# Performance work log

Measured on AMD Instinct MI355X. Metric: run time of the kernel, lower is better.

Reference implementation:

```python
import jax, jax.numpy as jnp
import numpy as np

BN_EPS = 1e-5


def setup_inputs() -> dict:
    key = jax.random.key(0)
    ks = jax.random.split(key, 12)
    B, C, N = 8, 256, 2048
    s = 1.0 / np.sqrt(C)
    x = jax.random.normal(ks[0], (B, C, N), dtype=jnp.float32)
    gamma = jnp.ones((C,), jnp.float32)
    beta = jnp.zeros((C,), jnp.float32)
    Wq = jax.random.normal(ks[1], (C, C), jnp.float32) * s
    bq = jnp.zeros((C,), jnp.float32)
    Wk = jax.random.normal(ks[2], (C, C), jnp.float32) * s
    bk = jnp.zeros((C,), jnp.float32)
    Wv = jax.random.normal(ks[3], (C, C), jnp.float32) * s
    bv = jnp.zeros((C,), jnp.float32)
    Wp = jax.random.normal(ks[4], (C, C), jnp.float32) * s
    bp = jnp.zeros((C,), jnp.float32)
    return {"x": x, "gamma": gamma, "beta": beta, "Wq": Wq, "bq": bq,
            "Wk": Wk, "bk": bk, "Wv": Wv, "bv": bv, "Wp": Wp, "bp": bp}


def reference(x, gamma, beta, Wq, bq, Wk, bk, Wv, bv, Wp, bp):
    B, C, N = x.shape
    # BatchNorm1d (training-mode batch stats): normalize per channel over (B, N)
    mean = jnp.mean(x, axis=(0, 2), keepdims=True)            # [1,C,1]
    var = jnp.mean(jnp.square(x - mean), axis=(0, 2), keepdims=True)
    h = (x - mean) * jax.lax.rsqrt(var + BN_EPS)
    h = h * gamma[None, :, None] + beta[None, :, None]
    # 1x1 Conv1d projections == per-position channel GEMMs
    q = jnp.einsum('oc,bcn->bno', Wq, h) + bq[None, None, :]  # [B,N,C]
    k = jnp.einsum('oc,bcn->bon', Wk, h) + bk[None, :, None]  # [B,C,N]
    v = jnp.einsum('oc,bcn->bno', Wv, h) + bv[None, None, :]  # [B,N,C]
    scale = jnp.asarray(C, x.dtype) ** -0.5
    w = jnp.einsum('bnc,bcm->bnm', q, k) * scale              # [B,N,N]
    w = jax.nn.softmax(w, axis=-1)
    h = jnp.einsum('bnm,bmc->bnc', w, v)                      # [B,N,C]
    out = jnp.einsum('oc,bnc->bon', Wp, h) + bp[None, :, None]  # [B,C,N]
    return x + out
```

## Files before the change

### kernel.cpp

```cpp
#include <hip/hip_runtime.h>
#include <hip/hip_fp16.h>

typedef _Float16 f16x8 __attribute__((ext_vector_type(8)));
typedef _Float16 f16x4 __attribute__((ext_vector_type(4)));
typedef float f32x4 __attribute__((ext_vector_type(4)));
typedef float f32x16 __attribute__((ext_vector_type(16)));

#define MFMA16(a, b, c) __builtin_amdgcn_mfma_f32_16x16x32_f16(a, b, c, 0, 0, 0)
#define MFMA32(a, b, c) __builtin_amdgcn_mfma_f32_32x32x16_f16(a, b, c, 0, 0, 0)

__device__ __forceinline__ void gload_lds16(const _Float16* g, void* l) {
    __builtin_amdgcn_global_load_lds(
        (const __attribute__((address_space(1))) void*)g,
        (__attribute__((address_space(3))) void*)l, 16, 0, 0);
}

__device__ __forceinline__ unsigned pkh(float a, float b) {
    typedef __fp16 fp16v2 __attribute__((ext_vector_type(2)));
    fp16v2 h = __builtin_amdgcn_cvt_pkrtz(a, b);
    return __builtin_bit_cast(unsigned, h);
}

__device__ __forceinline__ float fexp2(float x) {
#if __has_builtin(__builtin_amdgcn_exp2f)
    return __builtin_amdgcn_exp2f(x);
#else
    return exp2f(x);
#endif
}

__global__ __launch_bounds__(256) void prep_w_kernel(
    const float* __restrict__ Wq, const float* __restrict__ Wk,
    const float* __restrict__ Wv, const float* __restrict__ Wp,
    const float* __restrict__ bq, const float* __restrict__ bk,
    _Float16* __restrict__ out, float* __restrict__ bqk)
{
    int bid = blockIdx.x;
    int t = threadIdx.x;
    if (bid == 1024) {
        bqk[t]       = bq[t];
        bqk[256 + t] = bk[t];
        return;
    }
    int i = bid * 256 + t;
    int w = i >> 16, j = i & 65535;
    const float* src = (w == 0) ? Wq : (w == 1) ? Wk : (w == 2) ? Wv : Wp;
    out[i] = (_Float16)src[j];
}

__global__ __launch_bounds__(256) void bn_stats_kernel(
    const float* __restrict__ x, const float* __restrict__ gamma,
    const float* __restrict__ beta, float* __restrict__ scale,
    float* __restrict__ shift)
{
    int c = blockIdx.x, t = threadIdx.x;
    float s = 0.f, ss = 0.f;
    for (int b = 0; b < 8; ++b) {
        const float* p = x + ((size_t)b * 256 + c) * 2048;
        for (int n = t * 4; n < 2048; n += 1024) {
            float4 v = *(const float4*)(p + n);
            s  += v.x + v.y + v.z + v.w;
            ss += v.x*v.x + v.y*v.y + v.z*v.z + v.w*v.w;
        }
    }
    for (int off = 32; off > 0; off >>= 1) {
        s  += __shfl_down(s,  off, 64);
        ss += __shfl_down(ss, off, 64);
    }
    __shared__ float rs[4], rss[4];
    int w = t >> 6;
    if ((t & 63) == 0) { rs[w] = s; rss[w] = ss; }
    __syncthreads();
    if (t == 0) {
        float S  = rs[0] + rs[1] + rs[2] + rs[3];
        float SS = rss[0] + rss[1] + rss[2] + rss[3];
        float mean = S * (1.f / 16384.f);
        float var  = SS * (1.f / 16384.f) - mean * mean;
        float rstd = rsqrtf(var + 1e-5f);
        float sc = rstd * gamma[c];
        scale[c] = sc;
        shift[c] = beta[c] - mean * sc;
    }
}

__global__ __launch_bounds__(256) void norm_t_kernel(
    const float* __restrict__ x, const float* __restrict__ scale,
    const float* __restrict__ shift, _Float16* __restrict__ ht)
{
    __shared__ float tile[64][65];
    int t = threadIdx.x;
    int b = blockIdx.z, c0 = blockIdx.y * 64, n0 = blockIdx.x * 64;
    int nl = t & 63, cq = t >> 6;
#pragma unroll
    for (int r = 0; r < 16; ++r) {
        int cl = cq * 16 + r;
        float v = x[((size_t)b * 256 + c0 + cl) * 2048 + n0 + nl];
        tile[cl][nl] = v * scale[c0 + cl] + shift[c0 + cl];
    }
    __syncthreads();
    int cl2 = t & 63, nq = t >> 6;
#pragma unroll
    for (int r = 0; r < 16; ++r) {
        int nl2 = nq * 16 + r;
        ht[((size_t)b * 2048 + n0 + nl2) * 256 + c0 + cl2] = (_Float16)tile[cl2][nl2];
    }
}

template<int BN, int WGM, int WGN, typename OT, bool BIAS_I, bool RES>
__global__ __launch_bounds__(256, 3) void gemm_nt(
    const _Float16* __restrict__ Aall, long strideA,
    const _Float16* __restrict__ Ball, long strideB,
    const float* __restrict__ bias,
    const float* __restrict__ resid, long strideR,
    OT* __restrict__ Call, long strideC, int Nn)
{
    constexpr int BM = 128;
    constexpr int WR = BM / WGM;
    constexpr int WC = BN / WGN;
    constexpr int FM = WR / 16, FN = WC / 16;
    constexpr int BUFSZ = 8192 + BN * 64;
    constexpr int NI = 8 + BN / 16;
    constexpr int PW = NI / 4;

    int b = blockIdx.z;
    const _Float16* A  = Aall + (size_t)b * strideA;
    const _Float16* Bm = Ball + (size_t)b * strideB;
    OT* C = Call + (size_t)b * strideC;
    int i0 = blockIdx.y * BM, j0 = blockIdx.x * BN;

    __shared__ __align__(16) char lds[2 * BUFSZ];

    int t = threadIdx.x, lane = t & 63, w = t >> 6;
    int lr = lane & 15, lg = lane >> 4;
    int wm = w % WGM, wn = w / WGM;

    int soff = (lane >> 2) * 256 + (((lane & 3) ^ ((lane >> 3) & 3))) * 8;
    int lgx16 = ((lg ^ ((lr >> 1) & 3))) * 16;

    f32x4 acc[FM][FN] = {};

    auto stage = [&](int kk, int buf) {
#pragma unroll
        for (int i = 0; i < PW; ++i) {
            int u = w * PW + i;
            if (u < 8)
                gload_lds16(A + (size_t)(i0 + u * 16) * 256 + kk * 32 + soff,
                            lds + buf * BUFSZ + u * 1024);
            else
                gload_lds16(Bm + (size_t)(j0 + (u - 8) * 16) * 256 + kk * 32 + soff,
                            lds + buf * BUFSZ + 8192 + (u - 8) * 1024);
        }
    };

    stage(0, 0);
    __syncthreads();
    int buf = 0;
#pragma unroll
    for (int kk = 0; kk < 8; ++kk) {
        if (kk + 1 < 8) stage(kk + 1, buf ^ 1);
        const char* ab = lds + buf * BUFSZ;
        const char* bb = ab + 8192;
        f16x8 af[FM], bf[FN];
#pragma unroll
        for (int f = 0; f < FM; ++f)
            af[f] = *(const f16x8*)(ab + (wm * WR + f * 16 + lr) * 64 + lgx16);
#pragma unroll
        for (int f = 0; f < FN; ++f)
            bf[f] = *(const f16x8*)(bb + (wn * WC + f * 16 + lr) * 64 + lgx16);
        __builtin_amdgcn_s_setprio(1);
#pragma unroll
        for (int fm = 0; fm < FM; ++fm)
#pragma unroll
            for (int fn = 0; fn < FN; ++fn)
                acc[fm][fn] = MFMA16(af[fm], bf[fn], acc[fm][fn]);
        __builtin_amdgcn_s_setprio(0);
        __syncthreads();
        buf ^= 1;
    }
#pragma unroll
    for (int fm = 0; fm < FM; ++fm)
#pragma unroll
        for (int fn = 0; fn < FN; ++fn)
#pragma unroll
            for (int rr = 0; rr < 4; ++rr) {
                int row = i0 + wm * WR + fm * 16 + lg * 4 + rr;
                int col = j0 + wn * WC + fn * 16 + lr;
                float vv = acc[fm][fn][rr] + (BIAS_I ? bias[row] : bias[col]);
                if (RES) vv += resid[(size_t)b * strideR + (size_t)row * Nn + col];
                C[(size_t)row * Nn + col] = (OT)vv;
            }
}

__global__ __launch_bounds__(256, 2) void attn2_kernel(
    const _Float16* __restrict__ qk, const _Float16* __restrict__ vb,
    _Float16* __restrict__ Opart, float* __restrict__ mpart,
    float* __restrict__ lpart, int nsp, int mspan)
{
    int id = blockIdx.x;
    int b = id & 7;
    int rest = id >> 3;
    int qblk = rest & 15, sp = rest >> 4;
    int m_base = sp * mspan;
    int T = mspan >> 5;

    __shared__ __align__(16) char lds[66560];

    int t = threadIdx.x, ln = t & 63, w = t >> 6;
    int col = ln & 31, hi = ln >> 5;

    const _Float16* kg = qk + (size_t)b * 1048576 + 256;
    const _Float16* vg = vb + (size_t)b * 524288;

    int hsw = ((ln & 1) ^ ((ln >> 3) & 1));
    int koffs[4], voffs[4];
#pragma unroll
    for (int i = 0; i < 4; ++i) {
        int n = w * 4 + i;
        koffs[i] = (ln >> 1) * 512 + hsw * 8 + n * 16;
        voffs[i] = (((n & 7) * 32 + (ln >> 1)) * 2048) + ((n >> 3) * 16) + hsw * 8;
    }
    int frd = col * 32 + ((hi ^ ((col >> 2) & 1))) * 16;

    f16x8 qf[16];
    {
        const _Float16* qp = qk + ((size_t)b * 2048 + qblk * 128 + w * 32 + col) * 512 + hi * 8;
#pragma unroll
        for (int ks = 0; ks < 16; ++ks) {
            f16x8 v = *(const f16x8*)(qp + ks * 16);
#pragma unroll
            for (int e = 0; e < 8; ++e) v[e] = v[e] * (_Float16)0.09016844f;
            qf[ks] = v;
        }
    }

    f32x16 oacc[8] = {};
    float m_run = -1e30f, l_run = 0.f;

#pragma unroll
    for (int i = 0; i < 4; ++i) {
        int n = w * 4 + i;
        gload_lds16(kg + (size_t)m_base * 512 + koffs[i], lds + n * 1024);
        gload_lds16(vg + m_base + voffs[i], lds + 16384 + n * 1024);
    }
    __syncthreads();

    int buf = 0;
    for (int tt = 0; tt < T; ++tt) {
        if (tt + 1 < T) {
            int m0 = m_base + (tt + 1) * 32;
            char* kb = lds + (buf ^ 1) * 32768;
#pragma unroll
            for (int i = 0; i < 4; ++i) {
                int n = w * 4 + i;
                gload_lds16(kg + (size_t)m0 * 512 + koffs[i], kb + n * 1024);
                gload_lds16(vg + m0 + voffs[i], kb + 16384 + n * 1024);
            }
        }
        const char* kbase = lds + buf * 32768;
        const char* vbase = kbase + 16384;

        f32x16 s0 = {}, s1 = {};
        __builtin_amdgcn_s_setprio(1);
#pragma unroll
        for (int ks = 0; ks < 16; ks += 2) {
            f16x8 kf0 = *(const f16x8*)(kbase + ks * 1024 + frd);
            f16x8 kf1 = *(const f16x8*)(kbase + (ks + 1) * 1024 + frd);
            s0 = MFMA32(kf0, qf[ks], s0);
            s1 = MFMA32(kf1, qf[ks + 1], s1);
        }
        __builtin_amdgcn_s_setprio(0);
        f32x16 sacc = s0 + s1;

        float a0 = fmaxf(sacc[0], sacc[8]),  a1 = fmaxf(sacc[1], sacc[9]);
        float a2 = fmaxf(sacc[2], sacc[10]), a3 = fmaxf(sacc[3], sacc[11]);
        float a4 = fmaxf(sacc[4], sacc[12]), a5 = fmaxf(sacc[5], sacc[13]);
        float a6 = fmaxf(sacc[6], sacc[14]), a7 = fmaxf(sacc[7], sacc[15]);
        a0 = fmaxf(a0, a4); a1 = fmaxf(a1, a5); a2 = fmaxf(a2, a6); a3 = fmaxf(a3, a7);
        a0 = fmaxf(a0, a2); a1 = fmaxf(a1, a3);
        float rm = fmaxf(a0, a1);
        rm = fmaxf(rm, __shfl_xor(rm, 32, 64));

        if (__any(rm > m_run + 8.0f)) {
            float mnew = fmaxf(m_run, rm);
            float alpha = fexp2(m_run - mnew);
            l_run *= alpha;
#pragma unroll
            for (int dt = 0; dt < 8; ++dt) oacc[dt] *= alpha;
            m_run = mnew;
        }

        float pv_[16];
#pragma unroll
        for (int i = 0; i < 16; ++i) pv_[i] = fexp2(sacc[i] - m_run);
        float q0s = (pv_[0] + pv_[8])  + (pv_[1] + pv_[9]);
        float q1s = (pv_[2] + pv_[10]) + (pv_[3] + pv_[11]);
        float q2s = (pv_[4] + pv_[12]) + (pv_[5] + pv_[13]);
        float q3s = (pv_[6] + pv_[14]) + (pv_[7] + pv_[15]);
        float psum = (q0s + q1s) + (q2s + q3s);
        psum += __shfl_xor(psum, 32, 64);
        l_run += psum;

        unsigned W0[2], W1[2], W2[2], W3[2];
        W0[0] = pkh(pv_[0],  pv_[1]);  W0[1] = pkh(pv_[2],  pv_[3]);
        W1[0] = pkh(pv_[4],  pv_[5]);  W1[1] = pkh(pv_[6],  pv_[7]);
        W2[0] = pkh(pv_[8],  pv_[9]);  W2[1] = pkh(pv_[10], pv_[11]);
        W3[0] = pkh(pv_[12], pv_[13]); W3[1] = pkh(pv_[14], pv_[15]);

        __builtin_amdgcn_s_setprio(1);
#pragma unroll
        for (int j = 0; j < 2; ++j) {
            unsigned A0 = j ? W2[0] : W0[0], A1 = j ? W2[1] : W0[1];
            unsigned B0 = j ? W3[0] : W1[0], B1 = j ? W3[1] : W1[1];
            unsigned sx0 = hi ? A0 : B0, sx1 = hi ? A1 : B1;
            unsigned r0 = __shfl_xor(sx0, 32, 64), r1 = __shfl_xor(sx1, 32, 64);
            union { unsigned u[4]; f16x8 v; } pf;
            pf.u[0] = hi ? r0 : A0; pf.u[1] = hi ? r1 : A1;
            pf.u[2] = hi ? B0 : r0; pf.u[3] = hi ? B1 : r1;
#pragma unroll
            for (int dt = 0; dt < 8; ++dt) {
                f16x8 vf = *(const f16x8*)(vbase + j * 8192 + dt * 1024 + frd);
                oacc[dt] = MFMA32(vf, pf.v, oacc[dt]);
            }
        }
        __builtin_amdgcn_s_setprio(0);

        __syncthreads();
        buf ^= 1;
    }

    __syncthreads();
    _Float16* tr = (_Float16*)(lds + w * 16640);
    float invl = 1.0f / l_run;
#pragma unroll
    for (int dt = 0; dt < 8; ++dt)
#pragma unroll
        for (int g = 0; g < 4; ++g) {
            f16x4 q4;
#pragma unroll
            for (int e = 0; e < 4; ++e) q4[e] = (_Float16)(oacc[dt][g * 4 + e] * invl);
            int d0 = dt * 32 + g * 8 + 4 * hi;
            *(f16x4*)(tr + col * 260 + d0) = q4;
        }
    size_t region = ((size_t)((sp * 8 + b) * 16 + qblk)) * 32768;
    int rrow = ln >> 1, h = ln & 1;
    const _Float16* srcr = tr + rrow * 260 + h * 128;
    _Float16* dstr = Opart + region + (size_t)(w * 32 + rrow) * 256 + h * 128;
#pragma unroll
    for (int i = 0; i < 16; ++i)
        *(f16x8*)(dstr + i * 8) = *(const f16x8*)(srcr + i * 8);

    if (hi == 0) {
        int qi = w * 32 + col;
        int base = ((sp * 8 + b) * 16 + qblk) * 128 + qi;
        mpart[base] = m_run;
        lpart[base] = l_run;
    }
}

__global__ __launch_bounds__(256) void combine2_kernel(
    const _Float16* __restrict__ Opart, const float* __restrict__ mpart,
    const float* __restrict__ lpart, _Float16* __restrict__ abuf, int nsp)
{
    int id = blockIdx.x;
    int b = id & 7, qb = (id >> 3) & 15, dh = id >> 7;
    int t = threadIdx.x;
    __shared__ float cf[4][128];
    if (t < 128) {
        float m[4], l[4], mx = -1e30f;
        for (int sp = 0; sp < nsp; ++sp) {
            int base = ((sp * 8 + b) * 16 + qb) * 128 + t;
            m[sp] = mpart[base]; l[sp] = lpart[base];
            mx = fmaxf(mx, m[sp]);
        }
        float Wt = 0.f;
        for (int sp = 0; sp < nsp; ++sp) {
            float wv = l[sp] * fexp2(m[sp] - mx);
            cf[sp][t] = wv; Wt += wv;
        }
        float inv = 1.0f / Wt;
        for (int sp = 0; sp < nsp; ++sp) cf[sp][t] *= inv;
    }
    __syncthreads();
    size_t rb = ((size_t)(b * 16 + qb)) * 32768;
#pragma unroll
    for (int i = 0; i < 8; ++i) {
        int flat = i * 2048 + t * 8;
        int qi = flat >> 7, dl = flat & 127;
        float acc[8] = {};
        for (int sp = 0; sp < nsp; ++sp) {
            f16x8 v = *(const f16x8*)(Opart + (size_t)sp * 4194304 + rb +
                                      (size_t)qi * 256 + dh * 128 + dl);
            float c = cf[sp][qi];
#pragma unroll
            for (int e = 0; e < 8; ++e) acc[e] += c * (float)v[e];
        }
        f16x8 r;
#pragma unroll
        for (int e = 0; e < 8; ++e) r[e] = (_Float16)acc[e];
        *(f16x8*)(abuf + ((size_t)b * 2048 + qb * 128 + qi) * 256 + dh * 128 + dl) = r;
    }
}

extern "C" void kernel_launch(void* const* d_in, const int* in_sizes, int n_in,
                              void* d_out, int out_size, void* d_ws, size_t ws_size,
                              hipStream_t stream) {
    const float* x     = (const float*)d_in[0];
    const float* gamma = (const float*)d_in[1];
    const float* beta  = (const float*)d_in[2];
    const float* Wq    = (const float*)d_in[3];
    const float* bq    = (const float*)d_in[4];
    const float* Wk    = (const float*)d_in[5];
    const float* bk    = (const float*)d_in[6];
    const float* Wv    = (const float*)d_in[7];
    const float* bv    = (const float*)d_in[8];
    const float* Wp    = (const float*)d_in[9];
    const float* bp    = (const float*)d_in[10];
    float* out = (float*)d_out;

    char* ws = (char*)d_ws;
    float* scale = (float*)ws;
    float* shift = (float*)(ws + 1024);
    float* bqk   = (float*)(ws + 2048);
    float* mpart = (float*)(ws + 4096);
    float* lpart = (float*)(ws + 1052672);
    _Float16* wbf   = (_Float16*)(ws + 2101248);
    _Float16* Wvh   = wbf + 131072;
    _Float16* Wph   = wbf + 196608;
    _Float16* ht    = (_Float16*)(ws + 2625536);
    _Float16* qkbuf = (_Float16*)(ws + 11014144);
    _Float16* vbuf  = (_Float16*)(ws + 27791360);
    _Float16* Opart = (_Float16*)(ws + 36179968);
    _Float16* abuf  = ht;

    int nsp = (ws_size >= (size_t)36179968 + 4u * 8388608u) ? 4 : 2;
    int mspan = 2048 / nsp;

    const long SB = 524288;

    prep_w_kernel<<<1025, 256, 0, stream>>>(Wq, Wk, Wv, Wp, bq, bk, wbf, bqk);
    bn_stats_kernel<<<256, 256, 0, stream>>>(x, gamma, beta, scale, shift);
    norm_t_kernel<<<dim3(32, 4, 8), 256, 0, stream>>>(x, scale, shift, ht);
    gemm_nt<128, 2, 2, _Float16, false, false><<<dim3(4, 16, 8), 256, 0, stream>>>(
        ht, SB, wbf, 0, bqk, nullptr, 0, qkbuf, 1048576, 512);
    gemm_nt<64, 4, 1, _Float16, true, false><<<dim3(32, 2, 8), 256, 0, stream>>>(
        Wvh, 0, ht, SB, bv, nullptr, 0, vbuf, SB, 2048);
    attn2_kernel<<<128 * nsp, 256, 0, stream>>>(qkbuf, vbuf, Opart, mpart, lpart,
                                                nsp, mspan);
    combine2_kernel<<<256, 256, 0, stream>>>(Opart, mpart, lpart, abuf, nsp);
    gemm_nt<64, 4, 1, float, true, true><<<dim3(32, 2, 8), 256, 0, stream>>>(
        Wph, 0, abuf, SB, bp, x, SB, out, SB, 2048);
}
```

Before: 112.1 us.

## Rework attention pipeline: register-staged V, smaller LDS, 3 blocks/CU, up to 6 KV splits

The attention kernel now double-buffers only K in LDS through async global-to-LDS loads. V is prefetched into registers and written to a single LDS buffer after a barrier. This cuts LDS from 66.5KB to 48KB so launch bounds can target 3 blocks per CU, and the KV range can be split 6 ways when workspace allows. The PV MFMAs are interleaved with the exp computation for each half, the LDS swizzle is dropped, and the epilogue is done in two halves to fit the smaller LDS. Risks include bank conflicts from removing the swizzle, register pressure under the 3-block bound, and extra combine work with more splits.

```diff
diff --git a/kernel.cpp b/kernel.cpp
--- a/kernel.cpp
+++ b/kernel.cpp
@@ -191,19 +191,20 @@
             }
 }
 
-__global__ __launch_bounds__(256, 2) void attn2_kernel(
+__global__ __launch_bounds__(256, 3) void attn3_kernel(
     const _Float16* __restrict__ qk, const _Float16* __restrict__ vb,
     _Float16* __restrict__ Opart, float* __restrict__ mpart,
-    float* __restrict__ lpart, int nsp, int mspan)
+    float* __restrict__ lpart, int nsp)
 {
     int id = blockIdx.x;
     int b = id & 7;
     int rest = id >> 3;
     int qblk = rest & 15, sp = rest >> 4;
-    int m_base = sp * mspan;
-    int T = mspan >> 5;
-
-    __shared__ __align__(16) char lds[66560];
+    int t0 = (64 * sp) / nsp;
+    int t1 = (64 * (sp + 1)) / nsp;
+    int Tn = t1 - t0;
+
+    __shared__ __align__(16) char lds[49152];
 
     int t = threadIdx.x, ln = t & 63, w = t >> 6;
     int col = ln & 31, hi = ln >> 5;
@@ -211,15 +212,14 @@
     const _Float16* kg = qk + (size_t)b * 1048576 + 256;
     const _Float16* vg = vb + (size_t)b * 524288;
 
-    int hsw = ((ln & 1) ^ ((ln >> 3) & 1));
     int koffs[4], voffs[4];
 #pragma unroll
     for (int i = 0; i < 4; ++i) {
         int n = w * 4 + i;
-        koffs[i] = (ln >> 1) * 512 + hsw * 8 + n * 16;
-        voffs[i] = (((n & 7) * 32 + (ln >> 1)) * 2048) + ((n >> 3) * 16) + hsw * 8;
-    }
-    int frd = col * 32 + ((hi ^ ((col >> 2) & 1))) * 16;
+        koffs[i] = (ln >> 1) * 512 + (ln & 1) * 8 + n * 16;
+        voffs[i] = (((n & 7) * 32 + (ln >> 1)) * 2048) + ((n >> 3) * 16) + (ln & 1) * 8;
+    }
+    int frd = col * 32 + hi * 16;
 
     f16x8 qf[16];
     {
@@ -236,28 +236,41 @@
     f32x16 oacc[8] = {};
     float m_run = -1e30f, l_run = 0.f;
 
-#pragma unroll
-    for (int i = 0; i < 4; ++i) {
-        int n = w * 4 + i;
-        gload_lds16(kg + (size_t)m_base * 512 + koffs[i], lds + n * 1024);
-        gload_lds16(vg + m_base + voffs[i], lds + 16384 + n * 1024);
-    }
-    __syncthreads();
+    char* K0 = lds;
+    char* V  = lds + 32768;
+
+    {
+#pragma unroll
+        for (int i = 0; i < 4; ++i)
+            gload_lds16(kg + (size_t)(t0 * 32) * 512 + koffs[i], K0 + (w * 4 + i) * 1024);
+        int4 vr[4];
+#pragma unroll
+        for (int i = 0; i < 4; ++i)
+            vr[i] = *(const int4*)(vg + t0 * 32 + voffs[i]);
+#pragma unroll
+        for (int i = 0; i < 4; ++i)
+            *(int4*)(V + (w * 4 + i) * 1024 + ln * 16) = vr[i];
+        asm volatile("s_waitcnt vmcnt(0) lgkmcnt(0)" ::: "memory");
+        __builtin_amdgcn_sched_barrier(0);
+        if (Tn > 1) {
+#pragma unroll
+            for (int i = 0; i < 4; ++i)
+                gload_lds16(kg + (size_t)((t0 + 1) * 32) * 512 + koffs[i],
+                            K0 + 16384 + (w * 4 + i) * 1024);
+        }
+        __builtin_amdgcn_s_barrier();
+    }
 
     int buf = 0;
-    for (int tt = 0; tt < T; ++tt) {
-        if (tt + 1 < T) {
-            int m0 = m_base + (tt + 1) * 32;
-            char* kb = lds + (buf ^ 1) * 32768;
-#pragma unroll
-            for (int i = 0; i < 4; ++i) {
-                int n = w * 4 + i;
-                gload_lds16(kg + (size_t)m0 * 512 + koffs[i], kb + n * 1024);
-                gload_lds16(vg + m0 + voffs[i], kb + 16384 + n * 1024);
-            }
-        }
-        const char* kbase = lds + buf * 32768;
-        const char* vbase = kbase + 16384;
+    for (int tt = 0; tt < Tn; ++tt) {
+        int4 vr[4];
+        if (tt + 1 < Tn) {
+            int m0 = (t0 + tt + 1) * 32;
+#pragma unroll
+            for (int i = 0; i < 4; ++i)
+                vr[i] = *(const int4*)(vg + m0 + voffs[i]);
+        }
+        const char* kbase = lds + buf * 16384;
 
         f32x16 s0 = {}, s1 = {};
         __builtin_amdgcn_s_setprio(1);
@@ -289,65 +302,92 @@
             m_run = mnew;
         }
 
-        float pv_[16];
-#pragma unroll
-        for (int i = 0; i < 16; ++i) pv_[i] = fexp2(sacc[i] - m_run);
-        float q0s = (pv_[0] + pv_[8])  + (pv_[1] + pv_[9]);
-        float q1s = (pv_[2] + pv_[10]) + (pv_[3] + pv_[11]);
-        float q2s = (pv_[4] + pv_[12]) + (pv_[5] + pv_[13]);
-        float q3s = (pv_[6] + pv_[14]) + (pv_[7] + pv_[15]);
-        float psum = (q0s + q1s) + (q2s + q3s);
+        float pv0[8];
+#pragma unroll
+        for (int i = 0; i < 8; ++i) pv0[i] = fexp2(sacc[i] - m_run);
+        unsigned W0[2], W1[2];
+        W0[0] = pkh(pv0[0], pv0[1]); W0[1] = pkh(pv0[2], pv0[3]);
+        W1[0] = pkh(pv0[4], pv0[5]); W1[1] = pkh(pv0[6], pv0[7]);
+        {
+            unsigned sx0 = hi ? W0[0] : W1[0], sx1 = hi ? W0[1] : W1[1];
+            unsigned r0 = __shfl_xor(sx0, 32, 64), r1 = __shfl_xor(sx1, 32, 64);
+            union { unsigned u[4]; f16x8 v; } pf;
+            pf.u[0] = hi ? r0 : W0[0]; pf.u[1] = hi ? r1 : W0[1];
+            pf.u[2] = hi ? W1[0] : r0; pf.u[3] = hi ? W1[1] : r1;
+            __builtin_amdgcn_s_setprio(1);
+#pragma unroll
+            for (int dt = 0; dt < 8; ++dt) {
+                f16x8 vf = *(const f16x8*)(V + dt * 1024 + frd);
+                oacc[dt] = MFMA32(vf, pf.v, oacc[dt]);
+            }
+            __builtin_amdgcn_s_setprio(0);
+        }
+        float pv1[8];
+#pragma unroll
+        for (int i = 0; i < 8; ++i) pv1[i] = fexp2(sacc[8 + i] - m_run);
+        unsigned W2[2], W3[2];
+        W2[0] = pkh(pv1[0], pv1[1]); W2[1] = pkh(pv1[2], pv1[3]);
+        W3[0] = pkh(pv1[4], pv1[5]); W3[1] = pkh(pv1[6], pv1[7]);
+        {
+            unsigned sx0 = hi ? W2[0] : W3[0], sx1 = hi ? W2[1] : W3[1];
+            unsigned r0 = __shfl_xor(sx0, 32, 64), r1 = __shfl_xor(sx1, 32, 64);
+            union { unsigned u[4]; f16x8 v; } pf;
+            pf.u[0] = hi ? r0 : W2[0]; pf.u[1] = hi ? r1 : W2[1];
+            pf.u[2] = hi ? W3[0] : r0; pf.u[3] = hi ? W3[1] : r1;
+            __builtin_amdgcn_s_setprio(1);
+#pragma unroll
+            for (int dt = 0; dt < 8; ++dt) {
+                f16x8 vf = *(const f16x8*)(V + 8192 + dt * 1024 + frd);
+                oacc[dt] = MFMA32(vf, pf.v, oacc[dt]);
+            }
+            __builtin_amdgcn_s_setprio(0);
+        }
+        float psum = ((pv0[0]+pv0[1]) + (pv0[2]+pv0[3])) + ((pv0[4]+pv0[5]) + (pv0[6]+pv0[7]))
+                   + ((pv1[0]+pv1[1]) + (pv1[2]+pv1[3])) + ((pv1[4]+pv1[5]) + (pv1[6]+pv1[7]));
         psum += __shfl_xor(psum, 32, 64);
         l_run += psum;
 
-        unsigned W0[2], W1[2], W2[2], W3[2];
-        W0[0] = pkh(pv_[0],  pv_[1]);  W0[1] = pkh(pv_[2],  pv_[3]);
-        W1[0] = pkh(pv_[4],  pv_[5]);  W1[1] = pkh(pv_[6],  pv_[7]);
-        W2[0] = pkh(pv_[8],  pv_[9]);  W2[1] = pkh(pv_[10], pv_[11]);
-        W3[0] = pkh(pv_[12], pv_[13]); W3[1] = pkh(pv_[14], pv_[15]);
-
-        __builtin_amdgcn_s_setprio(1);
-#pragma unroll
-        for (int j = 0; j < 2; ++j) {
-            unsigned A0 = j ? W2[0] : W0[0], A1 = j ? W2[1] : W0[1];
-            unsigned B0 = j ? W3[0] : W1[0], B1 = j ? W3[1] : W1[1];
-            unsigned sx0 = hi ? A0 : B0, sx1 = hi ? A1 : B1;
-            unsigned r0 = __shfl_xor(sx0, 32, 64), r1 = __shfl_xor(sx1, 32, 64);
-            union { unsigned u[4]; f16x8 v; } pf;
-            pf.u[0] = hi ? r0 : A0; pf.u[1] = hi ? r1 : A1;
-            pf.u[2] = hi ? B0 : r0; pf.u[3] = hi ? B1 : r1;
-#pragma unroll
-            for (int dt = 0; dt < 8; ++dt) {
-                f16x8 vf = *(const f16x8*)(vbase + j * 8192 + dt * 1024 + frd);
-                oacc[dt] = MFMA32(vf, pf.v, oacc[dt]);
+        __builtin_amdgcn_s_barrier();
+        if (tt + 1 < Tn) {
+#pragma unroll
+            for (int i = 0; i < 4; ++i)
+                *(int4*)(V + (w * 4 + i) * 1024 + ln * 16) = vr[i];
+        }
+        asm volatile("s_waitcnt vmcnt(0) lgkmcnt(0)" ::: "memory");
+        __builtin_amdgcn_sched_barrier(0);
+        if (tt + 2 < Tn) {
+            int m0 = (t0 + tt + 2) * 32;
+#pragma unroll
+            for (int i = 0; i < 4; ++i)
+                gload_lds16(kg + (size_t)m0 * 512 + koffs[i],
+                            lds + buf * 16384 + (w * 4 + i) * 1024);
+        }
+        __builtin_amdgcn_s_barrier();
+        buf ^= 1;
+    }
+
+    _Float16* tr = (_Float16*)(lds + w * 8448);
+    float invl = 1.0f / l_run;
+    size_t region = ((size_t)((sp * 8 + b) * 16 + qblk)) * 32768;
+#pragma unroll
+    for (int dh2 = 0; dh2 < 2; ++dh2) {
+#pragma unroll
+        for (int dt4 = 0; dt4 < 4; ++dt4)
+#pragma unroll
+            for (int g = 0; g < 4; ++g) {
+                f16x4 q4;
+#pragma unroll
+                for (int e = 0; e < 4; ++e)
+                    q4[e] = (_Float16)(oacc[dh2 * 4 + dt4][g * 4 + e] * invl);
+                *(f16x4*)(tr + col * 132 + dt4 * 32 + g * 8 + 4 * hi) = q4;
             }
-        }
-        __builtin_amdgcn_s_setprio(0);
-
-        __syncthreads();
-        buf ^= 1;
-    }
-
-    __syncthreads();
-    _Float16* tr = (_Float16*)(lds + w * 16640);
-    float invl = 1.0f / l_run;
-#pragma unroll
-    for (int dt = 0; dt < 8; ++dt)
-#pragma unroll
-        for (int g = 0; g < 4; ++g) {
-            f16x4 q4;
-#pragma unroll
-            for (int e = 0; e < 4; ++e) q4[e] = (_Float16)(oacc[dt][g * 4 + e] * invl);
-            int d0 = dt * 32 + g * 8 + 4 * hi;
-            *(f16x4*)(tr + col * 260 + d0) = q4;
-        }
-    size_t region = ((size_t)((sp * 8 + b) * 16 + qblk)) * 32768;
-    int rrow = ln >> 1, h = ln & 1;
-    const _Float16* srcr = tr + rrow * 260 + h * 128;
-    _Float16* dstr = Opart + region + (size_t)(w * 32 + rrow) * 256 + h * 128;
-#pragma unroll
-    for (int i = 0; i < 16; ++i)
-        *(f16x8*)(dstr + i * 8) = *(const f16x8*)(srcr + i * 8);
+        int rrow = ln >> 1, h = ln & 1;
+        const _Float16* srcr = tr + rrow * 132 + h * 64;
+        _Float16* dstr = Opart + region + (size_t)(w * 32 + rrow) * 256 + dh2 * 128 + h * 64;
+#pragma unroll
+        for (int i = 0; i < 8; ++i)
+            *(f16x8*)(dstr + i * 8) = *(const f16x8*)(srcr + i * 8);
+    }
 
     if (hi == 0) {
         int qi = w * 32 + col;
@@ -364,9 +404,9 @@
     int id = blockIdx.x;
     int b = id & 7, qb = (id >> 3) & 15, dh = id >> 7;
     int t = threadIdx.x;
-    __shared__ float cf[4][128];
+    __shared__ float cf[8][128];
     if (t < 128) {
-        float m[4], l[4], mx = -1e30f;
+        float m[8], l[8], mx = -1e30f;
         for (int sp = 0; sp < nsp; ++sp) {
             int base = ((sp * 8 + b) * 16 + qb) * 128 + t;
             m[sp] = mpart[base]; l[sp] = lpart[base];
@@ -432,8 +472,9 @@
     _Float16* Opart = (_Float16*)(ws + 36179968);
     _Float16* abuf  = ht;
 
-    int nsp = (ws_size >= (size_t)36179968 + 4u * 8388608u) ? 4 : 2;
-    int mspan = 2048 / nsp;
+    int nsp = 2;
+    if (ws_size >= (size_t)36179968 + 6ull * 8388608ull)      nsp = 6;
+    else if (ws_size >= (size_t)36179968 + 4ull * 8388608ull) nsp = 4;
 
     const long SB = 524288;
 
@@ -444,8 +485,7 @@
         ht, SB, wbf, 0, bqk, nullptr, 0, qkbuf, 1048576, 512);
     gemm_nt<64, 4, 1, _Float16, true, false><<<dim3(32, 2, 8), 256, 0, stream>>>(
         Wvh, 0, ht, SB, bv, nullptr, 0, vbuf, SB, 2048);
-    attn2_kernel<<<128 * nsp, 256, 0, stream>>>(qkbuf, vbuf, Opart, mpart, lpart,
-                                                nsp, mspan);
+    attn3_kernel<<<128 * nsp, 256, 0, stream>>>(qkbuf, vbuf, Opart, mpart, lpart, nsp);
     combine2_kernel<<<256, 256, 0, stream>>>(Opart, mpart, lpart, abuf, nsp);
     gemm_nt<64, 4, 1, float, true, true><<<dim3(32, 2, 8), 256, 0, stream>>>(
         Wph, 0, abuf, SB, bp, x, SB, out, SB, 2048);
```

Measured after the change: 287.6 us. 2.57x slower.

## Software-pipeline attention: overlap next tile's QK^T with current PV MFMAs

Applied to the files above, without the earlier changes.

Restructures the attention inner loop so the QK^T score MFMAs for tile t+1 are interleaved with the PV MFMAs for tile t. The softmax for the next tile is computed after both. K and V loads are split and issued at different points, gated by explicit vmcnt waits and raw s_barriers. The aim is to keep the matrix units busy while exp and max work runs, and to hide LDS and global latency. The LDS XOR swizzle is removed, which may bring back bank conflicts, and the hand-written barrier and waitcnt choreography is fragile.

```diff
diff --git a/kernel.cpp b/kernel.cpp
--- a/kernel.cpp
+++ b/kernel.cpp
@@ -191,7 +191,7 @@
             }
 }
 
-__global__ __launch_bounds__(256, 2) void attn2_kernel(
+__global__ __launch_bounds__(256, 2) void attn4_kernel(
     const _Float16* __restrict__ qk, const _Float16* __restrict__ vb,
     _Float16* __restrict__ Opart, float* __restrict__ mpart,
     float* __restrict__ lpart, int nsp, int mspan)
@@ -211,15 +211,14 @@
     const _Float16* kg = qk + (size_t)b * 1048576 + 256;
     const _Float16* vg = vb + (size_t)b * 524288;
 
-    int hsw = ((ln & 1) ^ ((ln >> 3) & 1));
     int koffs[4], voffs[4];
 #pragma unroll
     for (int i = 0; i < 4; ++i) {
         int n = w * 4 + i;
-        koffs[i] = (ln >> 1) * 512 + hsw * 8 + n * 16;
-        voffs[i] = (((n & 7) * 32 + (ln >> 1)) * 2048) + ((n >> 3) * 16) + hsw * 8;
-    }
-    int frd = col * 32 + ((hi ^ ((col >> 2) & 1))) * 16;
+        koffs[i] = (ln >> 1) * 512 + (ln & 1) * 8 + n * 16;
+        voffs[i] = (((n & 7) * 32 + (ln >> 1)) * 2048) + ((n >> 3) * 16) + (ln & 1) * 8;
+    }
+    int frd = col * 32 + hi * 16;
 
     f16x8 qf[16];
     {
@@ -235,100 +234,160 @@
 
     f32x16 oacc[8] = {};
     float m_run = -1e30f, l_run = 0.f;
+    unsigned W[8];
 
 #pragma unroll
     for (int i = 0; i < 4; ++i) {
-        int n = w * 4 + i;
-        gload_lds16(kg + (size_t)m_base * 512 + koffs[i], lds + n * 1024);
-        gload_lds16(vg + m_base + voffs[i], lds + 16384 + n * 1024);
-    }
-    __syncthreads();
-
-    int buf = 0;
-    for (int tt = 0; tt < T; ++tt) {
-        if (tt + 1 < T) {
-            int m0 = m_base + (tt + 1) * 32;
-            char* kb = lds + (buf ^ 1) * 32768;
-#pragma unroll
-            for (int i = 0; i < 4; ++i) {
-                int n = w * 4 + i;
-                gload_lds16(kg + (size_t)m0 * 512 + koffs[i], kb + n * 1024);
-                gload_lds16(vg + m0 + voffs[i], kb + 16384 + n * 1024);
-            }
-        }
-        const char* kbase = lds + buf * 32768;
-        const char* vbase = kbase + 16384;
-
-        f32x16 s0 = {}, s1 = {};
+        gload_lds16(kg + (size_t)(m_base) * 512 + koffs[i], lds + (w * 4 + i) * 1024);
+        gload_lds16(vg + m_base + voffs[i], lds + 16384 + (w * 4 + i) * 1024);
+        gload_lds16(kg + (size_t)(m_base + 32) * 512 + koffs[i], lds + 32768 + (w * 4 + i) * 1024);
+        gload_lds16(vg + m_base + 32 + voffs[i], lds + 49152 + (w * 4 + i) * 1024);
+    }
+    asm volatile("s_waitcnt vmcnt(0)" ::: "memory");
+    __builtin_amdgcn_sched_barrier(0);
+    __builtin_amdgcn_s_barrier();
+    {
+        f32x16 sn = {};
         __builtin_amdgcn_s_setprio(1);
 #pragma unroll
-        for (int ks = 0; ks < 16; ks += 2) {
-            f16x8 kf0 = *(const f16x8*)(kbase + ks * 1024 + frd);
-            f16x8 kf1 = *(const f16x8*)(kbase + (ks + 1) * 1024 + frd);
-            s0 = MFMA32(kf0, qf[ks], s0);
-            s1 = MFMA32(kf1, qf[ks + 1], s1);
+        for (int ks = 0; ks < 16; ++ks) {
+            f16x8 kf = *(const f16x8*)(lds + ks * 1024 + frd);
+            sn = MFMA32(kf, qf[ks], sn);
         }
         __builtin_amdgcn_s_setprio(0);
-        f32x16 sacc = s0 + s1;
-
-        float a0 = fmaxf(sacc[0], sacc[8]),  a1 = fmaxf(sacc[1], sacc[9]);
-        float a2 = fmaxf(sacc[2], sacc[10]), a3 = fmaxf(sacc[3], sacc[11]);
-        float a4 = fmaxf(sacc[4], sacc[12]), a5 = fmaxf(sacc[5], sacc[13]);
-        float a6 = fmaxf(sacc[6], sacc[14]), a7 = fmaxf(sacc[7], sacc[15]);
+        float a0 = fmaxf(sn[0], sn[8]),  a1 = fmaxf(sn[1], sn[9]);
+        float a2 = fmaxf(sn[2], sn[10]), a3 = fmaxf(sn[3], sn[11]);
+        float a4 = fmaxf(sn[4], sn[12]), a5 = fmaxf(sn[5], sn[13]);
+        float a6 = fmaxf(sn[6], sn[14]), a7 = fmaxf(sn[7], sn[15]);
         a0 = fmaxf(a0, a4); a1 = fmaxf(a1, a5); a2 = fmaxf(a2, a6); a3 = fmaxf(a3, a7);
         a0 = fmaxf(a0, a2); a1 = fmaxf(a1, a3);
         float rm = fmaxf(a0, a1);
         rm = fmaxf(rm, __shfl_xor(rm, 32, 64));
-
-        if (__any(rm > m_run + 8.0f)) {
-            float mnew = fmaxf(m_run, rm);
-            float alpha = fexp2(m_run - mnew);
-            l_run *= alpha;
-#pragma unroll
-            for (int dt = 0; dt < 8; ++dt) oacc[dt] *= alpha;
-            m_run = mnew;
-        }
-
+        m_run = rm;
         float pv_[16];
 #pragma unroll
-        for (int i = 0; i < 16; ++i) pv_[i] = fexp2(sacc[i] - m_run);
-        float q0s = (pv_[0] + pv_[8])  + (pv_[1] + pv_[9]);
-        float q1s = (pv_[2] + pv_[10]) + (pv_[3] + pv_[11]);
-        float q2s = (pv_[4] + pv_[12]) + (pv_[5] + pv_[13]);
-        float q3s = (pv_[6] + pv_[14]) + (pv_[7] + pv_[15]);
-        float psum = (q0s + q1s) + (q2s + q3s);
+        for (int i = 0; i < 16; ++i) pv_[i] = fexp2(sn[i] - m_run);
+        float psum = ((pv_[0]+pv_[1]) + (pv_[2]+pv_[3])) + ((pv_[4]+pv_[5]) + (pv_[6]+pv_[7]))
+                   + ((pv_[8]+pv_[9]) + (pv_[10]+pv_[11])) + ((pv_[12]+pv_[13]) + (pv_[14]+pv_[15]));
         psum += __shfl_xor(psum, 32, 64);
-        l_run += psum;
-
-        unsigned W0[2], W1[2], W2[2], W3[2];
-        W0[0] = pkh(pv_[0],  pv_[1]);  W0[1] = pkh(pv_[2],  pv_[3]);
-        W1[0] = pkh(pv_[4],  pv_[5]);  W1[1] = pkh(pv_[6],  pv_[7]);
-        W2[0] = pkh(pv_[8],  pv_[9]);  W2[1] = pkh(pv_[10], pv_[11]);
-        W3[0] = pkh(pv_[12], pv_[13]); W3[1] = pkh(pv_[14], pv_[15]);
-
+        l_run = psum;
+        W[0] = pkh(pv_[0],  pv_[1]);  W[1] = pkh(pv_[2],  pv_[3]);
+        W[2] = pkh(pv_[4],  pv_[5]);  W[3] = pkh(pv_[6],  pv_[7]);
+        W[4] = pkh(pv_[8],  pv_[9]);  W[5] = pkh(pv_[10], pv_[11]);
+        W[6] = pkh(pv_[12], pv_[13]); W[7] = pkh(pv_[14], pv_[15]);
+    }
+    __builtin_amdgcn_s_barrier();
+
+    for (int tt = 0; tt < T - 1; ++tt) {
+        char* myb = lds + (tt & 1) * 32768;
+        char* nxb = lds + ((tt + 1) & 1) * 32768;
+        if (tt + 2 < T) {
+            int m0 = m_base + (tt + 2) * 32;
+#pragma unroll
+            for (int i = 0; i < 4; ++i)
+                gload_lds16(kg + (size_t)m0 * 512 + koffs[i], myb + (w * 4 + i) * 1024);
+        }
+        union { unsigned u[4]; f16x8 v; } pf0, pf1;
+        {
+            unsigned sx0 = hi ? W[0] : W[2], sx1 = hi ? W[1] : W[3];
+            unsigned r0 = __shfl_xor(sx0, 32, 64), r1 = __shfl_xor(sx1, 32, 64);
+            pf0.u[0] = hi ? r0 : W[0]; pf0.u[1] = hi ? r1 : W[1];
+            pf0.u[2] = hi ? W[2] : r0; pf0.u[3] = hi ? W[3] : r1;
+        }
+        {
+            unsigned sx0 = hi ? W[4] : W[6], sx1 = hi ? W[5] : W[7];
+            unsigned r0 = __shfl_xor(sx0, 32, 64), r1 = __shfl_xor(sx1, 32, 64);
+            pf1.u[0] = hi ? r0 : W[4]; pf1.u[1] = hi ? r1 : W[5];
+            pf1.u[2] = hi ? W[6] : r0; pf1.u[3] = hi ? W[7] : r1;
+        }
+        f32x16 sn = {};
         __builtin_amdgcn_s_setprio(1);
 #pragma unroll
-        for (int j = 0; j < 2; ++j) {
-            unsigned A0 = j ? W2[0] : W0[0], A1 = j ? W2[1] : W0[1];
-            unsigned B0 = j ? W3[0] : W1[0], B1 = j ? W3[1] : W1[1];
-            unsigned sx0 = hi ? A0 : B0, sx1 = hi ? A1 : B1;
+        for (int g = 0; g < 4; ++g) {
+#pragma unroll
+            for (int k2 = 0; k2 < 4; ++k2) {
+                int ks = g * 4 + k2;
+                f16x8 kf = *(const f16x8*)(nxb + ks * 1024 + frd);
+                sn = MFMA32(kf, qf[ks], sn);
+            }
+#pragma unroll
+            for (int k2 = 0; k2 < 4; ++k2) {
+                int idx = g * 4 + k2;
+                f16x8 vf = *(const f16x8*)(myb + 16384 + idx * 1024 + frd);
+                oacc[idx & 7] = MFMA32(vf, (g < 2) ? pf0.v : pf1.v, oacc[idx & 7]);
+            }
+        }
+        __builtin_amdgcn_s_setprio(0);
+        {
+            float a0 = fmaxf(sn[0], sn[8]),  a1 = fmaxf(sn[1], sn[9]);
+            float a2 = fmaxf(sn[2], sn[10]), a3 = fmaxf(sn[3], sn[11]);
+            float a4 = fmaxf(sn[4], sn[12]), a5 = fmaxf(sn[5], sn[13]);
+            float a6 = fmaxf(sn[6], sn[14]), a7 = fmaxf(sn[7], sn[15]);
+            a0 = fmaxf(a0, a4); a1 = fmaxf(a1, a5); a2 = fmaxf(a2, a6); a3 = fmaxf(a3, a7);
+            a0 = fmaxf(a0, a2); a1 = fmaxf(a1, a3);
+            float rm = fmaxf(a0, a1);
+            rm = fmaxf(rm, __shfl_xor(rm, 32, 64));
+            if (__any(rm > m_run + 8.0f)) {
+                float mnew = fmaxf(m_run, rm);
+                float alpha = fexp2(m_run - mnew);
+                l_run *= alpha;
+#pragma unroll
+                for (int dt = 0; dt < 8; ++dt) oacc[dt] *= alpha;
+                m_run = mnew;
+            }
+            float pv_[16];
+#pragma unroll
+            for (int i = 0; i < 16; ++i) pv_[i] = fexp2(sn[i] - m_run);
+            float psum = ((pv_[0]+pv_[1]) + (pv_[2]+pv_[3])) + ((pv_[4]+pv_[5]) + (pv_[6]+pv_[7]))
+                       + ((pv_[8]+pv_[9]) + (pv_[10]+pv_[11])) + ((pv_[12]+pv_[13]) + (pv_[14]+pv_[15]));
+            psum += __shfl_xor(psum, 32, 64);
+            l_run += psum;
+            W[0] = pkh(pv_[0],  pv_[1]);  W[1] = pkh(pv_[2],  pv_[3]);
+            W[2] = pkh(pv_[4],  pv_[5]);  W[3] = pkh(pv_[6],  pv_[7]);
+            W[4] = pkh(pv_[8],  pv_[9]);  W[5] = pkh(pv_[10], pv_[11]);
+            W[6] = pkh(pv_[12], pv_[13]); W[7] = pkh(pv_[14], pv_[15]);
+        }
+        __builtin_amdgcn_s_barrier();
+        __builtin_amdgcn_sched_barrier(0);
+        if (tt + 2 < T) {
+            int m0 = m_base + (tt + 2) * 32;
+#pragma unroll
+            for (int i = 0; i < 4; ++i)
+                gload_lds16(vg + m0 + voffs[i], myb + 16384 + (w * 4 + i) * 1024);
+        }
+        asm volatile("s_waitcnt vmcnt(4)" ::: "memory");
+        __builtin_amdgcn_sched_barrier(0);
+        __builtin_amdgcn_s_barrier();
+    }
+
+    asm volatile("s_waitcnt vmcnt(0)" ::: "memory");
+    __builtin_amdgcn_sched_barrier(0);
+    __builtin_amdgcn_s_barrier();
+    {
+        char* myb = lds + ((T - 1) & 1) * 32768;
+        union { unsigned u[4]; f16x8 v; } pf0, pf1;
+        {
+            unsigned sx0 = hi ? W[0] : W[2], sx1 = hi ? W[1] : W[3];
             unsigned r0 = __shfl_xor(sx0, 32, 64), r1 = __shfl_xor(sx1, 32, 64);
-            union { unsigned u[4]; f16x8 v; } pf;
-            pf.u[0] = hi ? r0 : A0; pf.u[1] = hi ? r1 : A1;
-            pf.u[2] = hi ? B0 : r0; pf.u[3] = hi ? B1 : r1;
-#pragma unroll
-            for (int dt = 0; dt < 8; ++dt) {
-                f16x8 vf = *(const f16x8*)(vbase + j * 8192 + dt * 1024 + frd);
-                oacc[dt] = MFMA32(vf, pf.v, oacc[dt]);
-            }
+            pf0.u[0] = hi ? r0 : W[0]; pf0.u[1] = hi ? r1 : W[1];
+            pf0.u[2] = hi ? W[2] : r0; pf0.u[3] = hi ? W[3] : r1;
+        }
+        {
+            unsigned sx0 = hi ? W[4] : W[6], sx1 = hi ? W[5] : W[7];
+            unsigned r0 = __shfl_xor(sx0, 32, 64), r1 = __shfl_xor(sx1, 32, 64);
+            pf1.u[0] = hi ? r0 : W[4]; pf1.u[1] = hi ? r1 : W[5];
+            pf1.u[2] = hi ? W[6] : r0; pf1.u[3] = hi ? W[7] : r1;
+        }
+        __builtin_amdgcn_s_setprio(1);
+#pragma unroll
+        for (int idx = 0; idx < 16; ++idx) {
+            f16x8 vf = *(const f16x8*)(myb + 16384 + idx * 1024 + frd);
+            oacc[idx & 7] = MFMA32(vf, (idx < 8) ? pf0.v : pf1.v, oacc[idx & 7]);
         }
         __builtin_amdgcn_s_setprio(0);
-
-        __syncthreads();
-        buf ^= 1;
-    }
-
-    __syncthreads();
+    }
+    __builtin_amdgcn_s_barrier();
+
     _Float16* tr = (_Float16*)(lds + w * 16640);
     float invl = 1.0f / l_run;
 #pragma unroll
@@ -444,7 +503,7 @@
         ht, SB, wbf, 0, bqk, nullptr, 0, qkbuf, 1048576, 512);
     gemm_nt<64, 4, 1, _Float16, true, false><<<dim3(32, 2, 8), 256, 0, stream>>>(
         Wvh, 0, ht, SB, bv, nullptr, 0, vbuf, SB, 2048);
-    attn2_kernel<<<128 * nsp, 256, 0, stream>>>(qkbuf, vbuf, Opart, mpart, lpart,
+    attn4_kernel<<<128 * nsp, 256, 0, stream>>>(qkbuf, vbuf, Opart, mpart, lpart,
                                                 nsp, mspan);
     combine2_kernel<<<256, 256, 0, stream>>>(Opart, mpart, lpart, abuf, nsp);
     gemm_nt<64, 4, 1, float, true, true><<<dim3(32, 2, 8), 256, 0, stream>>>(
```

Result: no change. 111.9 us (-0.1%).

## Load K/V fragments directly from global memory and fold Q scale into weights

Applied to the files above, without the earlier changes.

The attention kernel stops staging K and V tiles through double-buffered LDS with async global-to-LDS loads and barriers. Each wave now reads its MFMA fragments straight from global memory, relying on L2/L1 caching, since all four waves read the same K/V tiles. The softmax scale is folded into Wq and bq during weight prep, so the per-element Q scaling in the kernel goes away. This removes the block-wide barriers and LDS traffic but exposes global load latency with no explicit prefetch, and the four waves read K/V redundantly.

```diff
diff --git a/kernel.cpp b/kernel.cpp
--- a/kernel.cpp
+++ b/kernel.cpp
@@ -35,17 +35,20 @@
     const float* __restrict__ bq, const float* __restrict__ bk,
     _Float16* __restrict__ out, float* __restrict__ bqk)
 {
+    const float QS = 0.09016844f;
     int bid = blockIdx.x;
     int t = threadIdx.x;
     if (bid == 1024) {
-        bqk[t]       = bq[t];
+        bqk[t]       = bq[t] * QS;
         bqk[256 + t] = bk[t];
         return;
     }
     int i = bid * 256 + t;
     int w = i >> 16, j = i & 65535;
     const float* src = (w == 0) ? Wq : (w == 1) ? Wk : (w == 2) ? Wv : Wp;
-    out[i] = (_Float16)src[j];
+    float v = src[j];
+    if (w == 0) v *= QS;
+    out[i] = (_Float16)v;
 }
 
 __global__ __launch_bounds__(256) void bn_stats_kernel(
@@ -191,7 +194,7 @@
             }
 }
 
-__global__ __launch_bounds__(256, 2) void attn2_kernel(
+__global__ __launch_bounds__(256, 2) void attn5_kernel(
     const _Float16* __restrict__ qk, const _Float16* __restrict__ vb,
     _Float16* __restrict__ Opart, float* __restrict__ mpart,
     float* __restrict__ lpart, int nsp, int mspan)
@@ -208,73 +211,38 @@
     int t = threadIdx.x, ln = t & 63, w = t >> 6;
     int col = ln & 31, hi = ln >> 5;
 
-    const _Float16* kg = qk + (size_t)b * 1048576 + 256;
-    const _Float16* vg = vb + (size_t)b * 524288;
-
-    int hsw = ((ln & 1) ^ ((ln >> 3) & 1));
-    int koffs[4], voffs[4];
-#pragma unroll
-    for (int i = 0; i < 4; ++i) {
-        int n = w * 4 + i;
-        koffs[i] = (ln >> 1) * 512 + hsw * 8 + n * 16;
-        voffs[i] = (((n & 7) * 32 + (ln >> 1)) * 2048) + ((n >> 3) * 16) + hsw * 8;
-    }
-    int frd = col * 32 + ((hi ^ ((col >> 2) & 1))) * 16;
+    const _Float16* kfb = qk + (size_t)b * 1048576 + 256
+                        + (size_t)(m_base + col) * 512 + hi * 8;
+    const _Float16* vfb = vb + (size_t)b * 524288
+                        + (size_t)col * 2048 + m_base + hi * 8;
 
     f16x8 qf[16];
     {
         const _Float16* qp = qk + ((size_t)b * 2048 + qblk * 128 + w * 32 + col) * 512 + hi * 8;
 #pragma unroll
-        for (int ks = 0; ks < 16; ++ks) {
-            f16x8 v = *(const f16x8*)(qp + ks * 16);
-#pragma unroll
-            for (int e = 0; e < 8; ++e) v[e] = v[e] * (_Float16)0.09016844f;
-            qf[ks] = v;
-        }
+        for (int ks = 0; ks < 16; ++ks) qf[ks] = *(const f16x8*)(qp + ks * 16);
     }
 
     f32x16 oacc[8] = {};
     float m_run = -1e30f, l_run = 0.f;
 
-#pragma unroll
-    for (int i = 0; i < 4; ++i) {
-        int n = w * 4 + i;
-        gload_lds16(kg + (size_t)m_base * 512 + koffs[i], lds + n * 1024);
-        gload_lds16(vg + m_base + voffs[i], lds + 16384 + n * 1024);
-    }
-    __syncthreads();
-
-    int buf = 0;
     for (int tt = 0; tt < T; ++tt) {
-        if (tt + 1 < T) {
-            int m0 = m_base + (tt + 1) * 32;
-            char* kb = lds + (buf ^ 1) * 32768;
-#pragma unroll
-            for (int i = 0; i < 4; ++i) {
-                int n = w * 4 + i;
-                gload_lds16(kg + (size_t)m0 * 512 + koffs[i], kb + n * 1024);
-                gload_lds16(vg + m0 + voffs[i], kb + 16384 + n * 1024);
-            }
-        }
-        const char* kbase = lds + buf * 32768;
-        const char* vbase = kbase + 16384;
+        const _Float16* kt = kfb + (size_t)tt * 16384;
 
         f32x16 s0 = {}, s1 = {};
-        __builtin_amdgcn_s_setprio(1);
 #pragma unroll
         for (int ks = 0; ks < 16; ks += 2) {
-            f16x8 kf0 = *(const f16x8*)(kbase + ks * 1024 + frd);
-            f16x8 kf1 = *(const f16x8*)(kbase + (ks + 1) * 1024 + frd);
-            s0 = MFMA32(kf0, qf[ks], s0);
-            s1 = MFMA32(kf1, qf[ks + 1], s1);
-        }
-        __builtin_amdgcn_s_setprio(0);
-        f32x16 sacc = s0 + s1;
-
-        float a0 = fmaxf(sacc[0], sacc[8]),  a1 = fmaxf(sacc[1], sacc[9]);
-        float a2 = fmaxf(sacc[2], sacc[10]), a3 = fmaxf(sacc[3], sacc[11]);
-        float a4 = fmaxf(sacc[4], sacc[12]), a5 = fmaxf(sacc[5], sacc[13]);
-        float a6 = fmaxf(sacc[6], sacc[14]), a7 = fmaxf(sacc[7], sacc[15]);
+            f16x8 k0 = *(const f16x8*)(kt + ks * 16);
+            f16x8 k1 = *(const f16x8*)(kt + ks * 16 + 16);
+            s0 = MFMA32(k0, qf[ks], s0);
+            s1 = MFMA32(k1, qf[ks + 1], s1);
+        }
+        f32x16 sn = s0 + s1;
+
+        float a0 = fmaxf(sn[0], sn[8]),  a1 = fmaxf(sn[1], sn[9]);
+        float a2 = fmaxf(sn[2], sn[10]), a3 = fmaxf(sn[3], sn[11]);
+        float a4 = fmaxf(sn[4], sn[12]), a5 = fmaxf(sn[5], sn[13]);
+        float a6 = fmaxf(sn[6], sn[14]), a7 = fmaxf(sn[7], sn[15]);
         a0 = fmaxf(a0, a4); a1 = fmaxf(a1, a5); a2 = fmaxf(a2, a6); a3 = fmaxf(a3, a7);
         a0 = fmaxf(a0, a2); a1 = fmaxf(a1, a3);
         float rm = fmaxf(a0, a1);
@@ -291,12 +259,9 @@
 
         float pv_[16];
 #pragma unroll
-        for (int i = 0; i < 16; ++i) pv_[i] = fexp2(sacc[i] - m_run);
-        float q0s = (pv_[0] + pv_[8])  + (pv_[1] + pv_[9]);
-        float q1s = (pv_[2] + pv_[10]) + (pv_[3] + pv_[11]);
-        float q2s = (pv_[4] + pv_[12]) + (pv_[5] + pv_[13]);
-        float q3s = (pv_[6] + pv_[14]) + (pv_[7] + pv_[15]);
-        float psum = (q0s + q1s) + (q2s + q3s);
+        for (int i = 0; i < 16; ++i) pv_[i] = fexp2(sn[i] - m_run);
+        float psum = ((pv_[0]+pv_[1]) + (pv_[2]+pv_[3])) + ((pv_[4]+pv_[5]) + (pv_[6]+pv_[7]))
+                   + ((pv_[8]+pv_[9]) + (pv_[10]+pv_[11])) + ((pv_[12]+pv_[13]) + (pv_[14]+pv_[15]));
         psum += __shfl_xor(psum, 32, 64);
         l_run += psum;
 
@@ -306,29 +271,30 @@
         W2[0] = pkh(pv_[8],  pv_[9]);  W2[1] = pkh(pv_[10], pv_[11]);
         W3[0] = pkh(pv_[12], pv_[13]); W3[1] = pkh(pv_[14], pv_[15]);
 
-        __builtin_amdgcn_s_setprio(1);
-#pragma unroll
-        for (int j = 0; j < 2; ++j) {
-            unsigned A0 = j ? W2[0] : W0[0], A1 = j ? W2[1] : W0[1];
-            unsigned B0 = j ? W3[0] : W1[0], B1 = j ? W3[1] : W1[1];
-            unsigned sx0 = hi ? A0 : B0, sx1 = hi ? A1 : B1;
+        union { unsigned u[4]; f16x8 v; } pf0, pf1;
+        {
+            unsigned sx0 = hi ? W0[0] : W1[0], sx1 = hi ? W0[1] : W1[1];
             unsigned r0 = __shfl_xor(sx0, 32, 64), r1 = __shfl_xor(sx1, 32, 64);
-            union { unsigned u[4]; f16x8 v; } pf;
-            pf.u[0] = hi ? r0 : A0; pf.u[1] = hi ? r1 : A1;
-            pf.u[2] = hi ? B0 : r0; pf.u[3] = hi ? B1 : r1;
-#pragma unroll
-            for (int dt = 0; dt < 8; ++dt) {
-                f16x8 vf = *(const f16x8*)(vbase + j * 8192 + dt * 1024 + frd);
-                oacc[dt] = MFMA32(vf, pf.v, oacc[dt]);
-            }
-        }
-        __builtin_amdgcn_s_setprio(0);
-
-        __syncthreads();
-        buf ^= 1;
-    }
-
-    __syncthreads();
+            pf0.u[0] = hi ? r0 : W0[0]; pf0.u[1] = hi ? r1 : W0[1];
+            pf0.u[2] = hi ? W1[0] : r0; pf0.u[3] = hi ? W1[1] : r1;
+        }
+        {
+            unsigned sx0 = hi ? W2[0] : W3[0], sx1 = hi ? W2[1] : W3[1];
+            unsigned r0 = __shfl_xor(sx0, 32, 64), r1 = __shfl_xor(sx1, 32, 64);
+            pf1.u[0] = hi ? r0 : W2[0]; pf1.u[1] = hi ? r1 : W2[1];
+            pf1.u[2] = hi ? W3[0] : r0; pf1.u[3] = hi ? W3[1] : r1;
+        }
+
+        const _Float16* vt = vfb + tt * 32;
+#pragma unroll
+        for (int f = 0; f < 8; ++f) {
+            f16x8 v0 = *(const f16x8*)(vt + (size_t)f * 65536);
+            f16x8 v1 = *(const f16x8*)(vt + (size_t)f * 65536 + 16);
+            oacc[f] = MFMA32(v0, pf0.v, oacc[f]);
+            oacc[f] = MFMA32(v1, pf1.v, oacc[f]);
+        }
+    }
+
     _Float16* tr = (_Float16*)(lds + w * 16640);
     float invl = 1.0f / l_run;
 #pragma unroll
@@ -444,7 +410,7 @@
         ht, SB, wbf, 0, bqk, nullptr, 0, qkbuf, 1048576, 512);
     gemm_nt<64, 4, 1, _Float16, true, false><<<dim3(32, 2, 8), 256, 0, stream>>>(
         Wvh, 0, ht, SB, bv, nullptr, 0, vbuf, SB, 2048);
-    attn2_kernel<<<128 * nsp, 256, 0, stream>>>(qkbuf, vbuf, Opart, mpart, lpart,
+    attn5_kernel<<<128 * nsp, 256, 0, stream>>>(qkbuf, vbuf, Opart, mpart, lpart,
                                                 nsp, mspan);
     combine2_kernel<<<256, 256, 0, stream>>>(Opart, mpart, lpart, abuf, nsp);
     gemm_nt<64, 4, 1, float, true, true><<<dim3(32, 2, 8), 256, 0, stream>>>(
```

After: 185.9 us. 65.8% more time.
